# Kernel tuning notes

Measured on AMD Instinct MI355X. Metric: run time of the kernel, lower is better.

The kernel has to match this reference:

```python
import jax, jax.numpy as jnp
import numpy as np

N_NODES, N_EDGES, D_IN, D_OUT = 50000, 400000, 512, 512


def setup_inputs() -> dict:
    key = jax.random.key(0)
    k = jax.random.split(key, 7)
    s = 1.0 / np.sqrt(D_IN)
    return {
        "x": jax.random.normal(k[0], (N_NODES, D_IN), dtype=jnp.float32),
        "src": jax.random.randint(k[1], (N_EDGES,), 0, N_NODES),
        "dst": jax.random.randint(k[2], (N_EDGES,), 0, N_NODES),
        "W1": jax.random.uniform(k[3], (D_IN, D_OUT), jnp.float32, -s, s),
        "b1": jax.random.uniform(k[4], (D_OUT,), jnp.float32, -s, s),
        "W2": jax.random.uniform(k[5], (D_IN, D_OUT), jnp.float32, -s, s),
        "b2": jax.random.uniform(k[6], (D_OUT,), jnp.float32, -s, s),
    }


def reference(x, src, dst, W1, b1, W2, b2):
    n_nodes = x.shape[0]
    # gather src features along each edge, segment-sum into dst nodes
    msg_sum = jax.ops.segment_sum(x[src], dst, num_segments=n_nodes)      # [N, D_in]
    counts = jax.ops.segment_sum(jnp.ones_like(dst, dtype=x.dtype), dst,
                                 num_segments=n_nodes)                    # [N]
    mean = msg_sum / jnp.maximum(counts, 1.0)[:, None]                    # mailbox mean
    out = (x @ W1 + b1) + ((x - mean) @ W2 + b2)
    # DGL update_all leaves nodes with no incoming messages untouched
    return jnp.where((counts > 0)[:, None], out, x)
```

## Files before the change

### kernel.cpp

```cpp
#include <hip/hip_runtime.h>
#include <hip/hip_bf16.h>
#include <stdint.h>

typedef unsigned short u16;
typedef unsigned int   u32;

#define N_NODES 50000
#define N_EDGES 400000
#define DDIM    512
#define KTOT    1024
#define BM      128
#define BN      128
#define BK      64
#define NT      (KTOT / BK)
#define GRID_M  ((N_NODES + BM - 1) / BM)

typedef __attribute__((ext_vector_type(8))) __bf16 bf16x8;
typedef __attribute__((ext_vector_type(4))) float  f32x4;

__device__ __forceinline__ float bflo(u32 d) { return __builtin_bit_cast(float, d << 16); }
__device__ __forceinline__ float bfhi(u32 d) { return __builtin_bit_cast(float, d & 0xffff0000u); }
__device__ __forceinline__ u16 f2bf(float f) {
    u32 u = __builtin_bit_cast(u32, f);
    u32 r = u + 0x7fffu + ((u >> 16) & 1u);
    return (u16)(r >> 16);
}
__device__ __forceinline__ u32 pack2(float a, float b) {
    return (u32)f2bf(a) | ((u32)f2bf(b) << 16);
}
__device__ __forceinline__ void gload_lds16(const void* g, void* l) {
    __builtin_amdgcn_global_load_lds(
        (const __attribute__((address_space(1))) void*)g,
        (__attribute__((address_space(3))) void*)l, 16, 0, 0);
}

__global__ void cvt_k(const float* __restrict__ x, u16* __restrict__ Acat) {
    int i = blockIdx.x * 256 + threadIdx.x;
    int node = i >> 6, c8 = i & 63;
    const float4* p = (const float4*)(x + (size_t)node * DDIM + c8 * 8);
    float4 a = p[0], b = p[1];
    uint4 o;
    o.x = pack2(a.x, a.y); o.y = pack2(a.z, a.w);
    o.z = pack2(b.x, b.y); o.w = pack2(b.z, b.w);
    *(uint4*)(Acat + (size_t)node * KTOT + c8 * 8) = o;
}

__global__ void hist_k(const int* __restrict__ dst, int* __restrict__ counts) {
    int e = blockIdx.x * 256 + threadIdx.x;
    if (e < N_EDGES) atomicAdd(&counts[dst[e]], 1);
}

#define NCHUNK 49
__global__ __launch_bounds__(1024) void scanA_k(const int* __restrict__ counts, int* __restrict__ csum) {
    __shared__ int ws[16];
    int t = threadIdx.x, b = blockIdx.x;
    int i = b * 1024 + t;
    int v = (i < N_NODES) ? counts[i] : 0;
    for (int d = 32; d; d >>= 1) v += __shfl_down(v, d);
    if ((t & 63) == 0) ws[t >> 6] = v;
    __syncthreads();
    if (t < 16) {
        int s = ws[t];
        for (int d = 8; d; d >>= 1) s += __shfl_down(s, d);
        if (t == 0) csum[b] = s;
    }
}
__global__ void scanB_k(int* __restrict__ csum) {
    int t = threadIdx.x;
    int v = (t < NCHUNK) ? csum[t] : 0;
    int s = v;
    for (int d = 1; d < 64; d <<= 1) { int u = __shfl_up(s, d); if (t >= d) s += u; }
    if (t < NCHUNK) csum[t] = s - v;
}
__global__ __launch_bounds__(1024) void scanC_k(const int* __restrict__ counts, const int* __restrict__ csum,
                                                int* __restrict__ offsets, int* __restrict__ cursor) {
    __shared__ int wsum[16];
    int t = threadIdx.x, b = blockIdx.x;
    int i = b * 1024 + t;
    int lane = t & 63, w = t >> 6;
    int v = (i < N_NODES) ? counts[i] : 0;
    int s = v;
    for (int d = 1; d < 64; d <<= 1) { int u = __shfl_up(s, d); if (lane >= d) s += u; }
    if (lane == 63) wsum[w] = s;
    __syncthreads();
    if (t < 16) {
        int ww = wsum[t], ss = ww;
        for (int d = 1; d < 16; d <<= 1) { int u = __shfl_up(ss, d); if (t >= d) ss += u; }
        wsum[t] = ss - ww;
    }
    __syncthreads();
    int excl = (s - v) + wsum[w] + csum[b];
    if (i < N_NODES) { offsets[i] = excl; cursor[i] = excl; }
}

__global__ void fill_k(const int* __restrict__ src, const int* __restrict__ dst,
                       int* __restrict__ cursor, int* __restrict__ esrc) {
    int e = blockIdx.x * 256 + threadIdx.x;
    if (e < N_EDGES) {
        int d = dst[e];
        int p = atomicAdd(&cursor[d], 1);
        esrc[p] = src[e];
    }
}

__global__ void prepw_k(const float* __restrict__ W1, const float* __restrict__ W2,
                        const float* __restrict__ b1, const float* __restrict__ b2,
                        u16* __restrict__ Wcat, float* __restrict__ b12) {
    int idx = blockIdx.x * 256 + threadIdx.x;
    int k = idx >> 9, n = idx & 511;
    float w1 = W1[idx], w2 = W2[idx];
    Wcat[(size_t)n * KTOT + k]       = f2bf(w1 + w2);
    Wcat[(size_t)n * KTOT + 512 + k] = f2bf(w2);
    if (idx < 512) b12[idx] = b1[idx] + b2[idx];
}

__device__ __forceinline__ void addrow(float* acc, uint4 v) {
    acc[0] += bflo(v.x); acc[1] += bfhi(v.x);
    acc[2] += bflo(v.y); acc[3] += bfhi(v.y);
    acc[4] += bflo(v.z); acc[5] += bfhi(v.z);
    acc[6] += bflo(v.w); acc[7] += bfhi(v.w);
}
__global__ __launch_bounds__(256) void agg_k(u16* Acat,
                                             const int* __restrict__ offsets,
                                             const int* __restrict__ counts,
                                             const int* __restrict__ esrc) {
    int nid = blockIdx.x * 4 + (threadIdx.x >> 6);
    if (nid >= N_NODES) return;
    int lane = threadIdx.x & 63;
    int off = offsets[nid], deg = counts[nid];
    float acc[8] = {0, 0, 0, 0, 0, 0, 0, 0};
    int e = 0;
    for (; e + 3 < deg; e += 4) {
        int s0 = esrc[off + e], s1 = esrc[off + e + 1];
        int s2 = esrc[off + e + 2], s3 = esrc[off + e + 3];
        uint4 v0 = *(const uint4*)(Acat + (size_t)s0 * KTOT + lane * 8);
        uint4 v1 = *(const uint4*)(Acat + (size_t)s1 * KTOT + lane * 8);
        uint4 v2 = *(const uint4*)(Acat + (size_t)s2 * KTOT + lane * 8);
        uint4 v3 = *(const uint4*)(Acat + (size_t)s3 * KTOT + lane * 8);
        addrow(acc, v0); addrow(acc, v1); addrow(acc, v2); addrow(acc, v3);
    }
    for (; e < deg; e++) {
        int s0 = esrc[off + e];
        addrow(acc, *(const uint4*)(Acat + (size_t)s0 * KTOT + lane * 8));
    }
    float scale = (deg > 0) ? (-1.0f / (float)deg) : 0.0f;
    uint4 o;
    o.x = pack2(acc[0] * scale, acc[1] * scale);
    o.y = pack2(acc[2] * scale, acc[3] * scale);
    o.z = pack2(acc[4] * scale, acc[5] * scale);
    o.w = pack2(acc[6] * scale, acc[7] * scale);
    *(uint4*)(Acat + (size_t)nid * KTOT + 512 + lane * 8) = o;
}

__global__ __launch_bounds__(256, 2) void gemm_k(const u16* __restrict__ Acat,
                                                 const float* __restrict__ x,
                                                 const u16* __restrict__ Wcat,
                                                 const float* __restrict__ b12,
                                                 const int* __restrict__ counts,
                                                 float* __restrict__ out) {
    __shared__ u16 As[2][BM * BK];
    __shared__ u16 Bs[2][BN * BK];

    const int nwg = gridDim.x;
    int orig = blockIdx.x;
    int xcd = orig & 7, loc = orig >> 3;
    int q8 = nwg >> 3, r8 = nwg & 7;
    int wg = (xcd < r8 ? xcd * (q8 + 1) : r8 * (q8 + 1) + (xcd - r8) * q8) + loc;
    const int m0 = (wg >> 2) * BM;
    const int n0 = (wg & 3) * BN;

    const int tid  = threadIdx.x;
    const int lane = tid & 63;
    const int wid  = tid >> 6;
    const int wm = wid >> 1, wn = wid & 1;
    const int quad = lane >> 4, lr = lane & 15;

    const int srow = tid >> 3;
    const int so8  = (((tid & 7) ^ (srow & 7)) << 3);
    int arowg[4], browg[4];
    #pragma unroll
    for (int q = 0; q < 4; q++) {
        int r = q * 32 + srow;
        int ar = m0 + r; if (ar > N_NODES - 1) ar = N_NODES - 1;
        arowg[q] = ar;
        browg[q] = n0 + r;
    }

    f32x4 acc[4][4] = {};

    auto stage = [&](u16* Asb, u16* Bsb, int t) {
        const int k0 = t * BK;
        #pragma unroll
        for (int q = 0; q < 4; q++) {
            gload_lds16(Acat + (size_t)arowg[q] * KTOT + k0 + so8,
                        Asb + q * 2048 + wid * 512);
            gload_lds16(Wcat + (size_t)browg[q] * KTOT + k0 + so8,
                        Bsb + q * 2048 + wid * 512);
        }
    };

    const int swb   = (lr & 7) << 4;
    const int arow0 = (wm * 64 + lr) * 128;
    const int brow0 = (wn * 64 + lr) * 128;

    auto compute = [&](const u16* Asb, const u16* Bsb) {
        bf16x8 af[2][4], bfr[2][4];
        #pragma unroll
        for (int ks = 0; ks < 2; ks++) {
            const int koff = (ks * 64 + quad * 16) ^ swb;
            #pragma unroll
            for (int i = 0; i < 4; i++)
                af[ks][i] = *(const bf16x8*)((const char*)Asb + arow0 + i * 2048 + koff);
            #pragma unroll
            for (int j = 0; j < 4; j++)
                bfr[ks][j] = *(const bf16x8*)((const char*)Bsb + brow0 + j * 2048 + koff);
        }
        #pragma unroll
        for (int ks = 0; ks < 2; ks++)
            #pragma unroll
            for (int i = 0; i < 4; i++)
                #pragma unroll
                for (int j = 0; j < 4; j++)
                    acc[i][j] = __builtin_amdgcn_mfma_f32_16x16x32_bf16(af[ks][i], bfr[ks][j], acc[i][j], 0, 0, 0);
    };

    stage(As[0], Bs[0], 0);
    __syncthreads();
    #pragma unroll 1
    for (int t = 0; t < NT; t += 2) {
        stage(As[1], Bs[1], t + 1);
        compute(As[0], Bs[0]);
        __syncthreads();
        if (t + 2 < NT) stage(As[0], Bs[0], t + 2);
        compute(As[1], Bs[1]);
        __syncthreads();
    }

    #pragma unroll
    for (int i = 0; i < 4; i++) {
        #pragma unroll
        for (int r = 0; r < 4; r++) {
            int grow = m0 + wm * 64 + i * 16 + quad * 4 + r;
            if (grow >= N_NODES) continue;
            int cnt = counts[grow];
            #pragma unroll
            for (int j = 0; j < 4; j++) {
                int gcol = n0 + wn * 64 + j * 16 + lr;
                float v;
                if (cnt > 0) v = acc[i][j][r] + b12[gcol];
                else         v = x[(size_t)grow * DDIM + gcol];
                out[(size_t)grow * DDIM + gcol] = v;
            }
        }
    }
}

extern "C" void kernel_launch(void* const* d_in, const int* in_sizes, int n_in,
                              void* d_out, int out_size, void* d_ws, size_t ws_size,
                              hipStream_t stream) {
    const float* x  = (const float*)d_in[0];
    const int* src  = (const int*)d_in[1];
    const int* dst  = (const int*)d_in[2];
    const float* W1 = (const float*)d_in[3];
    const float* b1 = (const float*)d_in[4];
    const float* W2 = (const float*)d_in[5];
    const float* b2 = (const float*)d_in[6];
    float* out = (float*)d_out;

    char* ws = (char*)d_ws;
    size_t o = 0;
    auto alloc = [&](size_t bytes) { char* p = ws + o; o += (bytes + 255) & ~(size_t)255; return p; };
    int* counts   = (int*)alloc((size_t)N_NODES * 4);
    int* offsets  = (int*)alloc((size_t)N_NODES * 4);
    int* cursor   = (int*)alloc((size_t)N_NODES * 4);
    int* csum     = (int*)alloc((size_t)NCHUNK * 4);
    int* esrc     = (int*)alloc((size_t)N_EDGES * 4);
    u16* Wcat     = (u16*)alloc((size_t)512 * KTOT * 2);
    float* b12    = (float*)alloc((size_t)512 * 4);
    u16* Acat     = (u16*)alloc((size_t)N_NODES * KTOT * 2);
    (void)ws_size; (void)n_in; (void)in_sizes; (void)out_size;

    hipMemsetAsync(counts, 0, (size_t)N_NODES * 4, stream);
    cvt_k<<<(N_NODES * 64) / 256, 256, 0, stream>>>(x, Acat);
    hist_k<<<(N_EDGES + 255) / 256, 256, 0, stream>>>(dst, counts);
    scanA_k<<<NCHUNK, 1024, 0, stream>>>(counts, csum);
    scanB_k<<<1, 64, 0, stream>>>(csum);
    scanC_k<<<NCHUNK, 1024, 0, stream>>>(counts, csum, offsets, cursor);
    fill_k<<<(N_EDGES + 255) / 256, 256, 0, stream>>>(src, dst, cursor, esrc);
    prepw_k<<<(512 * 512) / 256, 256, 0, stream>>>(W1, W2, b1, b2, Wcat, b12);
    agg_k<<<(N_NODES + 3) / 4, 256, 0, stream>>>(Acat, offsets, counts, esrc);
    gemm_k<<<dim3(GRID_M * 4), 256, 0, stream>>>(Acat, x, Wcat, b12, counts, out);
}
```

Baseline: 417.2 us.

## Enlarge GEMM tile to 256x256 with 8 waves and interleaved LDS pipeline

The GEMM kernel moves from 128x128 tiles with 4 waves to 256x256 tiles with 8 waves (512 threads). The main loop is restructured so A and B tile loads are staged separately and interleaved between MFMA phases, with explicit vmcnt/lgkmcnt waits, barriers and s_setprio. The XCD remap is simplified to a formula that assumes the workgroup count divides by 8. The goal is more data reuse per LDS load and better overlap of memory and compute. In exchange there are fewer workgroups (about 392), higher register pressure from 32 accumulators per thread, possible occupancy loss, and a tile-mapping formula that is only correct when NWG is a multiple of 8.

```diff
diff --git a/kernel.cpp b/kernel.cpp
--- a/kernel.cpp
+++ b/kernel.cpp
@@ -9,11 +9,13 @@
 #define N_EDGES 400000
 #define DDIM    512
 #define KTOT    1024
-#define BM      128
-#define BN      128
+#define BM      256
+#define BN      256
 #define BK      64
 #define NT      (KTOT / BK)
-#define GRID_M  ((N_NODES + BM - 1) / BM)
+#define MTILES  ((N_NODES + BM - 1) / BM)
+#define NTILES  (DDIM / BN)
+#define NWG     (MTILES * NTILES)
 
 typedef __attribute__((ext_vector_type(8))) __bf16 bf16x8;
 typedef __attribute__((ext_vector_type(4))) float  f32x4;
@@ -152,7 +154,10 @@
     *(uint4*)(Acat + (size_t)nid * KTOT + 512 + lane * 8) = o;
 }
 
-__global__ __launch_bounds__(256, 2) void gemm_k(const u16* __restrict__ Acat,
+#define WAITLGKM() do { asm volatile("s_waitcnt lgkmcnt(0)" ::: "memory"); \
+                        __builtin_amdgcn_sched_barrier(0); } while (0)
+
+__global__ __launch_bounds__(512, 2) void gemm_k(const u16* __restrict__ Acat,
                                                  const float* __restrict__ x,
                                                  const u16* __restrict__ Wcat,
                                                  const float* __restrict__ b12,
@@ -161,86 +166,133 @@
     __shared__ u16 As[2][BM * BK];
     __shared__ u16 Bs[2][BN * BK];
 
-    const int nwg = gridDim.x;
-    int orig = blockIdx.x;
-    int xcd = orig & 7, loc = orig >> 3;
-    int q8 = nwg >> 3, r8 = nwg & 7;
-    int wg = (xcd < r8 ? xcd * (q8 + 1) : r8 * (q8 + 1) + (xcd - r8) * q8) + loc;
-    const int m0 = (wg >> 2) * BM;
-    const int n0 = (wg & 3) * BN;
+    const int tlin = (blockIdx.x & 7) * (NWG / 8) + (blockIdx.x >> 3);
+    const int m0 = (tlin >> 1) * BM;
+    const int n0 = (tlin & 1) * BN;
 
     const int tid  = threadIdx.x;
     const int lane = tid & 63;
     const int wid  = tid >> 6;
-    const int wm = wid >> 1, wn = wid & 1;
+    const int wm = wid >> 2, wn = wid & 3;
     const int quad = lane >> 4, lr = lane & 15;
 
-    const int srow = tid >> 3;
-    const int so8  = (((tid & 7) ^ (srow & 7)) << 3);
-    int arowg[4], browg[4];
+    const int so8u = (((tid & 7) ^ ((tid >> 3) & 7)) << 3);
+    int arowq[4], browq[4];
     #pragma unroll
     for (int q = 0; q < 4; q++) {
-        int r = q * 32 + srow;
+        int r = q * 64 + (tid >> 3);
         int ar = m0 + r; if (ar > N_NODES - 1) ar = N_NODES - 1;
-        arowg[q] = ar;
-        browg[q] = n0 + r;
-    }
-
-    f32x4 acc[4][4] = {};
-
-    auto stage = [&](u16* Asb, u16* Bsb, int t) {
+        arowq[q] = ar;
+        browq[q] = n0 + r;
+    }
+
+    auto stageA = [&](u16* A_c, int t) {
         const int k0 = t * BK;
         #pragma unroll
-        for (int q = 0; q < 4; q++) {
-            gload_lds16(Acat + (size_t)arowg[q] * KTOT + k0 + so8,
-                        Asb + q * 2048 + wid * 512);
-            gload_lds16(Wcat + (size_t)browg[q] * KTOT + k0 + so8,
-                        Bsb + q * 2048 + wid * 512);
+        for (int q = 0; q < 4; q++)
+            gload_lds16(Acat + (size_t)arowq[q] * KTOT + k0 + so8u,
+                        A_c + q * 4096 + wid * 512);
+    };
+    auto stageB = [&](u16* B_c, int t) {
+        const int k0 = t * BK;
+        #pragma unroll
+        for (int q = 0; q < 4; q++)
+            gload_lds16(Wcat + (size_t)browq[q] * KTOT + k0 + so8u,
+                        B_c + q * 4096 + wid * 512);
+    };
+
+    const int swb = (lr & 7) << 4;
+    auto ldA = [&](const u16* A_c, int mf, int ks) -> bf16x8 {
+        int row = wm * 128 + mf * 16 + lr;
+        return *(const bf16x8*)((const char*)A_c + row * 128 + ((ks * 64 + quad * 16) ^ swb));
+    };
+    auto ldB = [&](const u16* B_c, int nf, int ks) -> bf16x8 {
+        int row = wn * 64 + nf * 16 + lr;
+        return *(const bf16x8*)((const char*)B_c + row * 128 + ((ks * 64 + quad * 16) ^ swb));
+    };
+
+    f32x4 acc[8][4] = {};
+
+    stageA(As[0], 0); stageB(Bs[0], 0);
+    stageA(As[1], 1); stageB(Bs[1], 1);
+    asm volatile("s_waitcnt vmcnt(8)" ::: "memory");
+    __builtin_amdgcn_sched_barrier(0);
+    __builtin_amdgcn_s_barrier();
+
+    #pragma unroll 1
+    for (int t = 0; t < NT; ++t) {
+        u16* A_c = As[t & 1];
+        u16* B_c = Bs[t & 1];
+
+        bf16x8 bf0[4], bf1[4], af0[4];
+        #pragma unroll
+        for (int j = 0; j < 4; j++) bf0[j] = ldB(B_c, j, 0);
+        #pragma unroll
+        for (int j = 0; j < 4; j++) bf1[j] = ldB(B_c, j, 1);
+        #pragma unroll
+        for (int i = 0; i < 4; i++) af0[i] = ldA(A_c, i, 0);
+        __builtin_amdgcn_s_setprio(1);
+        #pragma unroll
+        for (int i = 0; i < 4; i++)
+            #pragma unroll
+            for (int j = 0; j < 4; j++)
+                acc[i][j] = __builtin_amdgcn_mfma_f32_16x16x32_bf16(af0[i], bf0[j], acc[i][j], 0, 0, 0);
+        __builtin_amdgcn_s_setprio(0);
+        WAITLGKM();
+        __builtin_amdgcn_s_barrier();
+
+        if (t + 2 < NT) stageB(B_c, t + 2);
+        bf16x8 af1[4];
+        #pragma unroll
+        for (int i = 0; i < 4; i++) af1[i] = ldA(A_c, 4 + i, 0);
+        __builtin_amdgcn_s_setprio(1);
+        #pragma unroll
+        for (int i = 0; i < 4; i++)
+            #pragma unroll
+            for (int j = 0; j < 4; j++)
+                acc[4 + i][j] = __builtin_amdgcn_mfma_f32_16x16x32_bf16(af1[i], bf0[j], acc[4 + i][j], 0, 0, 0);
+        __builtin_amdgcn_s_setprio(0);
+
+        bf16x8 af2[4], af3[4];
+        #pragma unroll
+        for (int i = 0; i < 4; i++) af2[i] = ldA(A_c, i, 1);
+        #pragma unroll
+        for (int i = 0; i < 4; i++) af3[i] = ldA(A_c, 4 + i, 1);
+        __builtin_amdgcn_s_setprio(1);
+        #pragma unroll
+        for (int i = 0; i < 4; i++)
+            #pragma unroll
+            for (int j = 0; j < 4; j++)
+                acc[i][j] = __builtin_amdgcn_mfma_f32_16x16x32_bf16(af2[i], bf1[j], acc[i][j], 0, 0, 0);
+        __builtin_amdgcn_s_setprio(0);
+        WAITLGKM();
+        __builtin_amdgcn_s_barrier();
+
+        if (t + 2 < NT) stageA(A_c, t + 2);
+        __builtin_amdgcn_s_setprio(1);
+        #pragma unroll
+        for (int i = 0; i < 4; i++)
+            #pragma unroll
+            for (int j = 0; j < 4; j++)
+                acc[4 + i][j] = __builtin_amdgcn_mfma_f32_16x16x32_bf16(af3[i], bf1[j], acc[4 + i][j], 0, 0, 0);
+        __builtin_amdgcn_s_setprio(0);
+
+        if (t < NT - 2) {
+            asm volatile("s_waitcnt vmcnt(8)" ::: "memory");
+            __builtin_amdgcn_sched_barrier(0);
+            __builtin_amdgcn_s_barrier();
+        } else if (t == NT - 2) {
+            asm volatile("s_waitcnt vmcnt(0)" ::: "memory");
+            __builtin_amdgcn_sched_barrier(0);
+            __builtin_amdgcn_s_barrier();
         }
-    };
-
-    const int swb   = (lr & 7) << 4;
-    const int arow0 = (wm * 64 + lr) * 128;
-    const int brow0 = (wn * 64 + lr) * 128;
-
-    auto compute = [&](const u16* Asb, const u16* Bsb) {
-        bf16x8 af[2][4], bfr[2][4];
-        #pragma unroll
-        for (int ks = 0; ks < 2; ks++) {
-            const int koff = (ks * 64 + quad * 16) ^ swb;
-            #pragma unroll
-            for (int i = 0; i < 4; i++)
-                af[ks][i] = *(const bf16x8*)((const char*)Asb + arow0 + i * 2048 + koff);
-            #pragma unroll
-            for (int j = 0; j < 4; j++)
-                bfr[ks][j] = *(const bf16x8*)((const char*)Bsb + brow0 + j * 2048 + koff);
-        }
-        #pragma unroll
-        for (int ks = 0; ks < 2; ks++)
-            #pragma unroll
-            for (int i = 0; i < 4; i++)
-                #pragma unroll
-                for (int j = 0; j < 4; j++)
-                    acc[i][j] = __builtin_amdgcn_mfma_f32_16x16x32_bf16(af[ks][i], bfr[ks][j], acc[i][j], 0, 0, 0);
-    };
-
-    stage(As[0], Bs[0], 0);
-    __syncthreads();
-    #pragma unroll 1
-    for (int t = 0; t < NT; t += 2) {
-        stage(As[1], Bs[1], t + 1);
-        compute(As[0], Bs[0]);
-        __syncthreads();
-        if (t + 2 < NT) stage(As[0], Bs[0], t + 2);
-        compute(As[1], Bs[1]);
-        __syncthreads();
     }
 
     #pragma unroll
-    for (int i = 0; i < 4; i++) {
+    for (int i = 0; i < 8; i++) {
         #pragma unroll
         for (int r = 0; r < 4; r++) {
-            int grow = m0 + wm * 64 + i * 16 + quad * 4 + r;
+            int grow = m0 + wm * 128 + i * 16 + quad * 4 + r;
             if (grow >= N_NODES) continue;
             int cnt = counts[grow];
             #pragma unroll
@@ -289,5 +341,5 @@
     fill_k<<<(N_EDGES + 255) / 256, 256, 0, stream>>>(src, dst, cursor, esrc);
     prepw_k<<<(512 * 512) / 256, 256, 0, stream>>>(W1, W2, b1, b2, Wcat, b12);
     agg_k<<<(N_NODES + 3) / 4, 256, 0, stream>>>(Acat, offsets, counts, esrc);
-    gemm_k<<<dim3(GRID_M * 4), 256, 0, stream>>>(Acat, x, Wcat, b12, counts, out);
-}
+    gemm_k<<<dim3(NWG), 512, 0, stream>>>(Acat, x, Wcat, b12, counts, out);
+}
```

New measurement: 407.9 us. 2.2% less time.

## Restructure GEMM to full-N 224x512 tiles with triple-buffered LDS pipeline

Applied to the files above, without the earlier changes.

The GEMM now gives each workgroup 224 rows and all 512 output columns, using 512 threads, a 7x8 MFMA fragment grid per wave and BK=32. Staging is triple-buffered with explicit vmcnt waits and one barrier per K step, and MFMA issue priority is raised. Because N is no longer split across workgroups, each A row is read from global memory once instead of four times, and the grid fits 50000 rows as 224 tiles, roughly one wave of workgroups. The aggregation loop also gains an 8-way unrolled gather to keep more loads in flight. The large accumulator array (56 f32x4 per thread) raises register pressure and could limit occupancy or cause spills.

```diff
diff --git a/kernel.cpp b/kernel.cpp
--- a/kernel.cpp
+++ b/kernel.cpp
@@ -9,14 +9,20 @@
 #define N_EDGES 400000
 #define DDIM    512
 #define KTOT    1024
-#define BM      128
-#define BN      128
-#define BK      64
+#define BM      224
+#define BMS     256
+#define BN      512
+#define BK      32
 #define NT      (KTOT / BK)
-#define GRID_M  ((N_NODES + BM - 1) / BM)
+#define MTILES  ((N_NODES + BM - 1) / BM)
 
 typedef __attribute__((ext_vector_type(8))) __bf16 bf16x8;
 typedef __attribute__((ext_vector_type(4))) float  f32x4;
+
+#define S_VMCNT(n) do { asm volatile("s_waitcnt vmcnt(" #n ")" ::: "memory"); \
+                        __builtin_amdgcn_sched_barrier(0); } while (0)
+#define S_LGKM0()  do { asm volatile("s_waitcnt lgkmcnt(0)" ::: "memory"); \
+                        __builtin_amdgcn_sched_barrier(0); } while (0)
 
 __device__ __forceinline__ float bflo(u32 d) { return __builtin_bit_cast(float, d << 16); }
 __device__ __forceinline__ float bfhi(u32 d) { return __builtin_bit_cast(float, d & 0xffff0000u); }
@@ -130,6 +136,17 @@
     int off = offsets[nid], deg = counts[nid];
     float acc[8] = {0, 0, 0, 0, 0, 0, 0, 0};
     int e = 0;
+    for (; e + 7 < deg; e += 8) {
+        int s[8];
+        #pragma unroll
+        for (int u = 0; u < 8; u++) s[u] = esrc[off + e + u];
+        uint4 v[8];
+        #pragma unroll
+        for (int u = 0; u < 8; u++)
+            v[u] = *(const uint4*)(Acat + (size_t)s[u] * KTOT + lane * 8);
+        #pragma unroll
+        for (int u = 0; u < 8; u++) addrow(acc, v[u]);
+    }
     for (; e + 3 < deg; e += 4) {
         int s0 = esrc[off + e], s1 = esrc[off + e + 1];
         int s2 = esrc[off + e + 2], s3 = esrc[off + e + 3];
@@ -152,100 +169,101 @@
     *(uint4*)(Acat + (size_t)nid * KTOT + 512 + lane * 8) = o;
 }
 
-__global__ __launch_bounds__(256, 2) void gemm_k(const u16* __restrict__ Acat,
+__global__ __launch_bounds__(512, 2) void gemm_k(const u16* __restrict__ Acat,
                                                  const float* __restrict__ x,
                                                  const u16* __restrict__ Wcat,
                                                  const float* __restrict__ b12,
                                                  const int* __restrict__ counts,
                                                  float* __restrict__ out) {
-    __shared__ u16 As[2][BM * BK];
-    __shared__ u16 Bs[2][BN * BK];
-
-    const int nwg = gridDim.x;
-    int orig = blockIdx.x;
-    int xcd = orig & 7, loc = orig >> 3;
-    int q8 = nwg >> 3, r8 = nwg & 7;
-    int wg = (xcd < r8 ? xcd * (q8 + 1) : r8 * (q8 + 1) + (xcd - r8) * q8) + loc;
-    const int m0 = (wg >> 2) * BM;
-    const int n0 = (wg & 3) * BN;
-
+    __shared__ u16 As[3][BMS * BK];
+    __shared__ u16 Bs[3][BN * BK];
+
+    const int m0 = blockIdx.x * BM;
     const int tid  = threadIdx.x;
     const int lane = tid & 63;
     const int wid  = tid >> 6;
-    const int wm = wid >> 1, wn = wid & 1;
+    const int wm = wid >> 2, wn = wid & 3;
     const int quad = lane >> 4, lr = lane & 15;
 
-    const int srow = tid >> 3;
-    const int so8  = (((tid & 7) ^ (srow & 7)) << 3);
-    int arowg[4], browg[4];
+    const int srl   = tid >> 2;
+    const int ssoff = (((tid & 3) ^ (srl & 3)) << 3);
+    int arow[2];
     #pragma unroll
-    for (int q = 0; q < 4; q++) {
-        int r = q * 32 + srow;
-        int ar = m0 + r; if (ar > N_NODES - 1) ar = N_NODES - 1;
-        arowg[q] = ar;
-        browg[q] = n0 + r;
-    }
-
-    f32x4 acc[4][4] = {};
-
-    auto stage = [&](u16* Asb, u16* Bsb, int t) {
+    for (int q = 0; q < 2; q++) {
+        int r = m0 + q * 128 + srl;
+        arow[q] = (r < N_NODES) ? r : (N_NODES - 1);
+    }
+
+    auto stage = [&](int t) {
+        u16* A_c = As[t % 3]; u16* B_c = Bs[t % 3];
         const int k0 = t * BK;
         #pragma unroll
-        for (int q = 0; q < 4; q++) {
-            gload_lds16(Acat + (size_t)arowg[q] * KTOT + k0 + so8,
-                        Asb + q * 2048 + wid * 512);
-            gload_lds16(Wcat + (size_t)browg[q] * KTOT + k0 + so8,
-                        Bsb + q * 2048 + wid * 512);
+        for (int q = 0; q < 2; q++)
+            gload_lds16(Acat + (size_t)arow[q] * KTOT + k0 + ssoff,
+                        A_c + q * 4096 + wid * 512);
+        #pragma unroll
+        for (int q = 0; q < 4; q++)
+            gload_lds16(Wcat + (size_t)(q * 128 + srl) * KTOT + k0 + ssoff,
+                        B_c + q * 4096 + wid * 512);
+    };
+
+    const int rsw = (lr & 3);
+    auto ldA = [&](const u16* A_c, int mf) -> bf16x8 {
+        int row = wm * 112 + mf * 16 + lr;
+        return *(const bf16x8*)((const char*)A_c + row * 64 + ((quad ^ rsw) << 4));
+    };
+    auto ldB = [&](const u16* B_c, int nf) -> bf16x8 {
+        int row = wn * 128 + nf * 16 + lr;
+        return *(const bf16x8*)((const char*)B_c + row * 64 + ((quad ^ rsw) << 4));
+    };
+
+    f32x4 acc[7][8] = {};
+
+    stage(0); stage(1);
+    S_VMCNT(6);
+    __builtin_amdgcn_s_barrier();
+
+    #pragma unroll 1
+    for (int t = 0; t < NT; ++t) {
+        const u16* A_c = As[t % 3];
+        const u16* B_c = Bs[t % 3];
+
+        bf16x8 af[7], bf[8];
+        #pragma unroll
+        for (int i = 0; i < 7; i++) af[i] = ldA(A_c, i);
+        #pragma unroll
+        for (int j = 0; j < 8; j++) bf[j] = ldB(B_c, j);
+
+        if (t + 2 < NT) stage(t + 2);
+
+        __builtin_amdgcn_s_setprio(1);
+        #pragma unroll
+        for (int i = 0; i < 7; i++)
+            #pragma unroll
+            for (int j = 0; j < 8; j++)
+                acc[i][j] = __builtin_amdgcn_mfma_f32_16x16x32_bf16(af[i], bf[j], acc[i][j], 0, 0, 0);
+        __builtin_amdgcn_s_setprio(0);
+
+        S_LGKM0();
+        if (t < NT - 2) {
+            S_VMCNT(6);
+            __builtin_amdgcn_s_barrier();
+        } else if (t == NT - 2) {
+            S_VMCNT(0);
+            __builtin_amdgcn_s_barrier();
         }
-    };
-
-    const int swb   = (lr & 7) << 4;
-    const int arow0 = (wm * 64 + lr) * 128;
-    const int brow0 = (wn * 64 + lr) * 128;
-
-    auto compute = [&](const u16* Asb, const u16* Bsb) {
-        bf16x8 af[2][4], bfr[2][4];
-        #pragma unroll
-        for (int ks = 0; ks < 2; ks++) {
-            const int koff = (ks * 64 + quad * 16) ^ swb;
-            #pragma unroll
-            for (int i = 0; i < 4; i++)
-                af[ks][i] = *(const bf16x8*)((const char*)Asb + arow0 + i * 2048 + koff);
-            #pragma unroll
-            for (int j = 0; j < 4; j++)
-                bfr[ks][j] = *(const bf16x8*)((const char*)Bsb + brow0 + j * 2048 + koff);
-        }
-        #pragma unroll
-        for (int ks = 0; ks < 2; ks++)
-            #pragma unroll
-            for (int i = 0; i < 4; i++)
-                #pragma unroll
-                for (int j = 0; j < 4; j++)
-                    acc[i][j] = __builtin_amdgcn_mfma_f32_16x16x32_bf16(af[ks][i], bfr[ks][j], acc[i][j], 0, 0, 0);
-    };
-
-    stage(As[0], Bs[0], 0);
-    __syncthreads();
-    #pragma unroll 1
-    for (int t = 0; t < NT; t += 2) {
-        stage(As[1], Bs[1], t + 1);
-        compute(As[0], Bs[0]);
-        __syncthreads();
-        if (t + 2 < NT) stage(As[0], Bs[0], t + 2);
-        compute(As[1], Bs[1]);
-        __syncthreads();
     }
 
     #pragma unroll
-    for (int i = 0; i < 4; i++) {
+    for (int i = 0; i < 7; i++) {
         #pragma unroll
         for (int r = 0; r < 4; r++) {
-            int grow = m0 + wm * 64 + i * 16 + quad * 4 + r;
+            int grow = m0 + wm * 112 + i * 16 + quad * 4 + r;
             if (grow >= N_NODES) continue;
             int cnt = counts[grow];
             #pragma unroll
-            for (int j = 0; j < 4; j++) {
-                int gcol = n0 + wn * 64 + j * 16 + lr;
+            for (int j = 0; j < 8; j++) {
+                int gcol = wn * 128 + j * 16 + lr;
                 float v;
                 if (cnt > 0) v = acc[i][j][r] + b12[gcol];
                 else         v = x[(size_t)grow * DDIM + gcol];
@@ -289,5 +307,5 @@
     fill_k<<<(N_EDGES + 255) / 256, 256, 0, stream>>>(src, dst, cursor, esrc);
     prepw_k<<<(512 * 512) / 256, 256, 0, stream>>>(W1, W2, b1, b2, Wcat, b12);
     agg_k<<<(N_NODES + 3) / 4, 256, 0, stream>>>(Acat, offsets, counts, esrc);
-    gemm_k<<<dim3(GRID_M * 4), 256, 0, stream>>>(Acat, x, Wcat, b12, counts, out);
-}
+    gemm_k<<<dim3(MTILES), 512, 0, stream>>>(Acat, x, Wcat, b12, counts, out);
+}
```

Result: slower. 572.7 us (+37.3%).
